# Kernel tuning notes

Hardware: AMD Instinct MI355X
Metric: run time of the kernel (lower is better)

Reference implementation:

```python
import jax, jax.numpy as jnp
import numpy as np

BATCH = 262144
N_STEPS = 10  # hard-coded `range(10)` in the original get_cycles


def _euler_to_matrix(e):
    # Standard extrinsic xyz convention: R = Rz(z) @ Ry(y) @ Rx(x)
    x, y, z = e[..., 0], e[..., 1], e[..., 2]
    cx, sx = jnp.cos(x), jnp.sin(x)
    cy, sy = jnp.cos(y), jnp.sin(y)
    cz, sz = jnp.cos(z), jnp.sin(z)
    r0 = jnp.stack([cz * cy, cz * sy * sx - sz * cx, cz * sy * cx + sz * sx], -1)
    r1 = jnp.stack([sz * cy, sz * sy * sx + cz * cx, sz * sy * cx - cz * sx], -1)
    r2 = jnp.stack([-sy, cy * sx, cy * cx], -1)
    return jnp.stack([r0, r1, r2], -2)  # (..., 3, 3)


def _matrix_to_euler(R):
    # Classic rotationMatrixToEulerAngles (inverse of Rz@Ry@Rx), with singular branch
    sy = jnp.sqrt(R[..., 0, 0] ** 2 + R[..., 1, 0] ** 2)
    singular = sy < 1e-6
    x = jnp.where(singular,
                  jnp.arctan2(-R[..., 1, 2], R[..., 1, 1]),
                  jnp.arctan2(R[..., 2, 1], R[..., 2, 2]))
    y = jnp.arctan2(-R[..., 2, 0], sy)
    z = jnp.where(singular, jnp.zeros_like(sy), jnp.arctan2(R[..., 1, 0], R[..., 0, 0]))
    return jnp.stack([x, y, z], -1)


def _get_cycles(x):
    # x: (B, 6*N_STEPS), interleaved [t(3), r(3)] per step (per the original reshape())
    x = jax.lax.stop_gradient(x)  # mirrors .detach().numpy() in the original
    g = x.reshape(x.shape[0], N_STEPS, 6)
    t = g[:, :, :3]   # (B, S, 3) translations
    r = g[:, :, 3:]   # (B, S, 3) euler rotations

    # --- translation part ---
    # The original aliases path_pred[0] onto t[0:3] via .numpy() and mutates it
    # in-place across cycle iterations (j=0 doubles it). The resulting recorded
    # values obey: v_0 = t_0 ; v_i = 2*v_{i-1} + sum_{j=1}^{i-1} t_j
    C = jnp.cumsum(t[:, 1:, :], axis=1)  # C[:, k-1, :] = sum_{j=1..k} t_j
    v = [t[:, 0, :]]
    for i in range(1, N_STEPS):
        tail = C[:, i - 2, :] if i >= 2 else jnp.zeros_like(v[0])
        v.append(2.0 * v[-1] + tail)
    trans = jnp.stack(v, axis=1)  # (B, S, 3)

    # --- rotation part ---
    # numpy `*=` is ELEMENTWISE, so cycle i records
    # matrix_to_euler( R(r_1) * prod_{j<i} R(r_j) )  (Hadamard product)
    R = _euler_to_matrix(r)                    # (B, S, 3, 3)
    CP = jnp.cumprod(R, axis=1)                # CP[:, k] = elemwise prod_{j<=k} R_j
    P = jnp.concatenate([jnp.ones_like(R[:, :1]), CP[:, :-1]], axis=1)  # prod_{j<i}
    M = R[:, 1:2] * P                          # (B, S, 3, 3)
    rot = _matrix_to_euler(M)                  # (B, S, 3)

    return jnp.stack([trans, rot], axis=2)     # (B, S, 2, 3)


def setup_inputs():
    key = jax.random.key(0)
    k1, k2 = jax.random.split(key)
    pred = jax.random.normal(k1, (BATCH, 6 * N_STEPS), dtype=jnp.float32)
    gt = jax.random.normal(k2, (BATCH, 6 * N_STEPS), dtype=jnp.float32)
    return {"pred": pred, "gt": gt}


def reference(pred, gt):
    pred_cycles = _get_cycles(pred)
    gt_cycles = _get_cycles(gt)
    loss = jnp.mean((pred_cycles - gt_cycles) ** 2)
    return loss / BATCH  # original divides the MSE by self.batch_size
```

## Files before the change

### kernel.cpp

```cpp
#include <hip/hip_runtime.h>
#include <math.h>

#define NSTEP 10

__device__ __forceinline__ float fast_atan2f(float y, float x) {
    float ax = fabsf(x), ay = fabsf(y);
    float mx = fmaxf(ax, ay);
    float mn = fminf(ax, ay);
    float a = mn * __builtin_amdgcn_rcpf(mx);
    float s = a * a;
    float r = fmaf(s, fmaf(s, 0.0793312f, -0.2886793f), 0.9953545f) * a;
    if (ay > ax) r = 1.57079632679f - r;
    if (x < 0.0f) r = 3.14159265359f - r;
    return copysignf(r, y);
}

__device__ __forceinline__ void euler2mat5(float x, float y, float z, float R[5]) {
    float sx, cx, sy, cy, sz, cz;
    __sincosf(x, &sx, &cx);
    __sincosf(y, &sy, &cy);
    __sincosf(z, &sz, &cz);
    R[0] = cz * cy;
    R[1] = sz * cy;
    R[2] = -sy;
    R[3] = cy * sx;
    R[4] = cy * cx;
}

__device__ __forceinline__ void emit(float v, float& acc) {
    int pi = __builtin_amdgcn_update_dpp(0, __float_as_int(v), 0xB1, 0xF, 0xF, true);
    float d = v - __int_as_float(pi);
    acc = fmaf(d, d, acc);
}

__device__ __forceinline__ void emit_euler(const float M[5], float& acc) {
    float sy = __builtin_amdgcn_sqrtf(fmaf(M[0], M[0], M[1] * M[1]));
    emit(fast_atan2f(M[3], M[4]), acc);
    emit(fast_atan2f(-M[2], sy), acc);
    emit(fast_atan2f(M[1], M[0]), acc);
}

__global__ __launch_bounds__(256, 8) void cycle_loss_main(
    const float* __restrict__ pred, const float* __restrict__ gt,
    float* __restrict__ partial)
{
    const int tid  = threadIdx.x;
    const int lane = tid & 63;
    const int wid  = tid >> 6;

    const size_t sample = (size_t)blockIdx.x * 128 + (tid >> 1);
    const float* bp = (tid & 1) ? gt : pred;
    const float4* rp = reinterpret_cast<const float4*>(bp + sample * 60);

    float acc = 0.0f;
    float v[3], cac[3] = {0.f, 0.f, 0.f}, tprev[3], Q[5];

    float4 A = rp[0], B = rp[1], C = rp[2];

    {
        float4 nA = rp[3], nB = rp[4], nC = rp[5];
        float e0 = A.x, e1 = A.y, e2 = A.z, e3 = A.w,
              e4 = B.x, e5 = B.y, e6 = B.z, e7 = B.w,
              e8 = C.x, e9 = C.y, e10 = C.z, e11 = C.w;

        v[0] = e0; v[1] = e1; v[2] = e2;
        emit(v[0], acc); emit(v[1], acc); emit(v[2], acc);
        #pragma unroll
        for (int k = 0; k < 3; ++k) { v[k] *= 2.0f; emit(v[k], acc); }
        tprev[0] = e6; tprev[1] = e7; tprev[2] = e8;

        float R1[5];
        euler2mat5(e3, e4, e5, Q);
        euler2mat5(e9, e10, e11, R1);
        emit_euler(R1, acc);
        #pragma unroll
        for (int k = 0; k < 5; ++k) Q[k] *= R1[k];
        emit_euler(Q, acc);
        #pragma unroll
        for (int k = 0; k < 5; ++k) Q[k] *= R1[k];

        A = nA; B = nB; C = nC;
    }

    #pragma unroll
    for (int c = 1; c < 5; ++c) {
        float4 nA, nB, nC;
        if (c < 4) { nA = rp[3*c + 3]; nB = rp[3*c + 4]; nC = rp[3*c + 5]; }
        float f0 = A.x, f1 = A.y, f2 = A.z, f3 = A.w,
              f4 = B.x, f5 = B.y, f6 = B.z, f7 = B.w,
              f8 = C.x, f9 = C.y, f10 = C.z, f11 = C.w;
        (void)f4; (void)f5;

        cac[0] += tprev[0]; cac[1] += tprev[1]; cac[2] += tprev[2];
        #pragma unroll
        for (int k = 0; k < 3; ++k) { v[k] = fmaf(2.0f, v[k], cac[k]); emit(v[k], acc); }
        cac[0] += f0; cac[1] += f1; cac[2] += f2;
        #pragma unroll
        for (int k = 0; k < 3; ++k) { v[k] = fmaf(2.0f, v[k], cac[k]); emit(v[k], acc); }
        tprev[0] = f6; tprev[1] = f7; tprev[2] = f8;

        emit_euler(Q, acc);
        {
            float R[5];
            euler2mat5(f3, f4, f5, R);
            #pragma unroll
            for (int k = 0; k < 5; ++k) Q[k] *= R[k];
        }
        emit_euler(Q, acc);
        if (c < 4) {
            float R[5];
            euler2mat5(f9, f10, f11, R);
            #pragma unroll
            for (int k = 0; k < 5; ++k) Q[k] *= R[k];
            A = nA; B = nB; C = nC;
        }
    }

    #pragma unroll
    for (int off = 32; off > 0; off >>= 1)
        acc += __shfl_down(acc, off, 64);
    if (lane == 0)
        partial[blockIdx.x * 4 + wid] = acc;
}

__global__ __launch_bounds__(256) void cycle_loss_fin(
    const float* __restrict__ partial, float* __restrict__ out,
    int nparts, float inv)
{
    int t = threadIdx.x;
    float s = 0.0f;
    for (int i = t; i < nparts; i += 256) s += partial[i];
    int lane = t & 63, wid = t >> 6;
    #pragma unroll
    for (int off = 32; off > 0; off >>= 1)
        s += __shfl_down(s, off, 64);
    __shared__ float warp_s[4];
    if (lane == 0) warp_s[wid] = s;
    __syncthreads();
    if (t == 0)
        out[0] = (warp_s[0] + warp_s[1] + warp_s[2] + warp_s[3]) * inv;
}

extern "C" void kernel_launch(void* const* d_in, const int* in_sizes, int n_in,
                              void* d_out, int out_size, void* d_ws, size_t ws_size,
                              hipStream_t stream) {
    const float* pred = (const float*)d_in[0];
    const float* gt   = (const float*)d_in[1];
    int batch = in_sizes[0] / 60;
    float* partial = (float*)d_ws;

    const int threads = 256;
    const int blocks = batch / 128;
    cycle_loss_main<<<blocks, threads, 0, stream>>>(pred, gt, partial);

    double inv = 0.5 / (60.0 * (double)batch * (double)batch);
    cycle_loss_fin<<<1, threads, 0, stream>>>(partial, (float*)d_out, blocks * 4, (float)inv);
}
```

Before: 153.7 us.

## Fuse main and finalize kernels via cooperative launch with grid sync

```diff
diff --git a/kernel.cpp b/kernel.cpp
--- a/kernel.cpp
+++ b/kernel.cpp
@@ -1,5 +1,8 @@
 #include <hip/hip_runtime.h>
+#include <hip/hip_cooperative_groups.h>
 #include <math.h>
+
+namespace cg = cooperative_groups;
 
 #define NSTEP 10
 
@@ -40,19 +43,14 @@
     emit(fast_atan2f(M[1], M[0]), acc);
 }
 
-__global__ __launch_bounds__(256, 8) void cycle_loss_main(
+__device__ __forceinline__ void do_work(
     const float* __restrict__ pred, const float* __restrict__ gt,
-    float* __restrict__ partial)
+    int w, int tid, float& acc)
 {
-    const int tid  = threadIdx.x;
-    const int lane = tid & 63;
-    const int wid  = tid >> 6;
-
-    const size_t sample = (size_t)blockIdx.x * 128 + (tid >> 1);
+    const size_t sample = (size_t)w * 128 + (tid >> 1);
     const float* bp = (tid & 1) ? gt : pred;
     const float4* rp = reinterpret_cast<const float4*>(bp + sample * 60);
 
-    float acc = 0.0f;
     float v[3], cac[3] = {0.f, 0.f, 0.f}, tprev[3], Q[5];
 
     float4 A = rp[0], B = rp[1], C = rp[2];
@@ -62,6 +60,7 @@
         float e0 = A.x, e1 = A.y, e2 = A.z, e3 = A.w,
               e4 = B.x, e5 = B.y, e6 = B.z, e7 = B.w,
               e8 = C.x, e9 = C.y, e10 = C.z, e11 = C.w;
+        (void)e4; (void)e5;
 
         v[0] = e0; v[1] = e1; v[2] = e2;
         emit(v[0], acc); emit(v[1], acc); emit(v[2], acc);
@@ -115,30 +114,44 @@
             A = nA; B = nB; C = nC;
         }
     }
+}
+
+__global__ __launch_bounds__(256, 8) void cycle_loss_fused(
+    const float* __restrict__ pred, const float* __restrict__ gt,
+    float* __restrict__ partial, float* __restrict__ out,
+    int nwork, float inv)
+{
+    const int tid  = threadIdx.x;
+    const int lane = tid & 63;
+    const int wid  = tid >> 6;
+
+    float acc = 0.0f;
+    for (int w = blockIdx.x; w < nwork; w += gridDim.x)
+        do_work(pred, gt, w, tid, acc);
 
     #pragma unroll
     for (int off = 32; off > 0; off >>= 1)
         acc += __shfl_down(acc, off, 64);
-    if (lane == 0)
-        partial[blockIdx.x * 4 + wid] = acc;
-}
+    __shared__ float wsum[4];
+    __shared__ float wsum2[4];
+    if (lane == 0) wsum[wid] = acc;
+    __syncthreads();
+    if (tid == 0)
+        partial[blockIdx.x] = wsum[0] + wsum[1] + wsum[2] + wsum[3];
 
-__global__ __launch_bounds__(256) void cycle_loss_fin(
-    const float* __restrict__ partial, float* __restrict__ out,
-    int nparts, float inv)
-{
-    int t = threadIdx.x;
-    float s = 0.0f;
-    for (int i = t; i < nparts; i += 256) s += partial[i];
-    int lane = t & 63, wid = t >> 6;
-    #pragma unroll
-    for (int off = 32; off > 0; off >>= 1)
-        s += __shfl_down(s, off, 64);
-    __shared__ float warp_s[4];
-    if (lane == 0) warp_s[wid] = s;
-    __syncthreads();
-    if (t == 0)
-        out[0] = (warp_s[0] + warp_s[1] + warp_s[2] + warp_s[3]) * inv;
+    cg::this_grid().sync();
+
+    if (blockIdx.x == 0) {
+        float s = 0.0f;
+        for (int i = tid; i < (int)gridDim.x; i += 256) s += partial[i];
+        #pragma unroll
+        for (int off = 32; off > 0; off >>= 1)
+            s += __shfl_down(s, off, 64);
+        if (lane == 0) wsum2[wid] = s;
+        __syncthreads();
+        if (tid == 0)
+            out[0] = (wsum2[0] + wsum2[1] + wsum2[2] + wsum2[3]) * inv;
+    }
 }
 
 extern "C" void kernel_launch(void* const* d_in, const int* in_sizes, int n_in,
@@ -147,12 +160,26 @@
     const float* pred = (const float*)d_in[0];
     const float* gt   = (const float*)d_in[1];
     int batch = in_sizes[0] / 60;
+    int nwork = batch / 128;
     float* partial = (float*)d_ws;
+    float* outp = (float*)d_out;
 
-    const int threads = 256;
-    const int blocks = batch / 128;
-    cycle_loss_main<<<blocks, threads, 0, stream>>>(pred, gt, partial);
+    static int maxblk = 0;
+    if (maxblk == 0) {
+        int perCU = 0, ncu = 0;
+        hipOccupancyMaxActiveBlocksPerMultiprocessor(
+            &perCU, reinterpret_cast<const void*>(cycle_loss_fused), 256, 0);
+        hipDeviceGetAttribute(&ncu, hipDeviceAttributeMultiprocessorCount, 0);
+        if (perCU < 1) perCU = 1;
+        if (ncu < 1) ncu = 256;
+        maxblk = perCU * ncu;
+    }
+    int blocks = maxblk < nwork ? maxblk : nwork;
 
-    double inv = 0.5 / (60.0 * (double)batch * (double)batch);
-    cycle_loss_fin<<<1, threads, 0, stream>>>(partial, (float*)d_out, blocks * 4, (float)inv);
+    float inv = (float)(0.5 / (60.0 * (double)batch * (double)batch));
+
+    void* args[] = { (void*)&pred, (void*)&gt, (void*)&partial,
+                     (void*)&outp, (void*)&nwork, (void*)&inv };
+    hipLaunchCooperativeKernel(reinterpret_cast<void*>(cycle_loss_fused),
+                               dim3(blocks), dim3(256), args, 0, stream);
 }
```

New measurement: 314.2 us. 104% more time.

## Stage sample rows into LDS via coalesced global_load_lds with one-wave blocks

Applied to the files above, without the earlier changes.

```diff
diff --git a/kernel.cpp b/kernel.cpp
--- a/kernel.cpp
+++ b/kernel.cpp
@@ -2,6 +2,11 @@
 #include <math.h>
 
 #define NSTEP 10
+#define TILE_DW   3840
+#define GT_DW     1920
+
+#define GV (const __attribute__((address_space(1))) void*)
+#define LV (__attribute__((address_space(3))) void*)
 
 __device__ __forceinline__ float fast_atan2f(float y, float x) {
     float ax = fabsf(x), ay = fabsf(y);
@@ -40,25 +45,38 @@
     emit(fast_atan2f(M[1], M[0]), acc);
 }
 
-__global__ __launch_bounds__(256, 8) void cycle_loss_main(
+__global__ __launch_bounds__(64, 4) void cycle_loss_main(
     const float* __restrict__ pred, const float* __restrict__ gt,
     float* __restrict__ partial)
 {
-    const int tid  = threadIdx.x;
-    const int lane = tid & 63;
-    const int wid  = tid >> 6;
+    __shared__ float lds[TILE_DW];
+    const int lane = threadIdx.x;
 
-    const size_t sample = (size_t)blockIdx.x * 128 + (tid >> 1);
-    const float* bp = (tid & 1) ? gt : pred;
-    const float4* rp = reinterpret_cast<const float4*>(bp + sample * 60);
+    {
+        const size_t base = (size_t)blockIdx.x * 32 * 60;
+        const float* pg = pred + base;
+        const float* gg = gt   + base;
+
+        #pragma unroll
+        for (int it = 0; it < 15; ++it) {
+            const int d = it * 256 + lane * 4;
+            const float* src = (d < GT_DW) ? (pg + d) : (gg + (d - GT_DW));
+            __builtin_amdgcn_global_load_lds(GV src, LV(lds + it * 256), 16, 0, 0);
+        }
+        asm volatile("s_waitcnt vmcnt(0)" ::: "memory");
+        __builtin_amdgcn_sched_barrier(0);
+    }
 
     float acc = 0.0f;
-    float v[3], cac[3] = {0.f, 0.f, 0.f}, tprev[3], Q[5];
+    {
+        const float* row = lds + ((lane & 1) ? GT_DW : 0) + (lane >> 1) * 60;
 
-    float4 A = rp[0], B = rp[1], C = rp[2];
+        float v[3], cac[3] = {0,0,0}, tprev[3];
+        float Q[5];
 
-    {
-        float4 nA = rp[3], nB = rp[4], nC = rp[5];
+        float4 A = *reinterpret_cast<const float4*>(row);
+        float4 B = *reinterpret_cast<const float4*>(row + 4);
+        float4 C = *reinterpret_cast<const float4*>(row + 8);
         float e0 = A.x, e1 = A.y, e2 = A.z, e3 = A.w,
               e4 = B.x, e5 = B.y, e6 = B.z, e7 = B.w,
               e8 = C.x, e9 = C.y, e10 = C.z, e11 = C.w;
@@ -69,50 +87,50 @@
         for (int k = 0; k < 3; ++k) { v[k] *= 2.0f; emit(v[k], acc); }
         tprev[0] = e6; tprev[1] = e7; tprev[2] = e8;
 
-        float R1[5];
-        euler2mat5(e3, e4, e5, Q);
-        euler2mat5(e9, e10, e11, R1);
-        emit_euler(R1, acc);
+        {
+            float R1[5];
+            euler2mat5(e3, e4, e5, Q);
+            euler2mat5(e9, e10, e11, R1);
+            emit_euler(R1, acc);
+            #pragma unroll
+            for (int k = 0; k < 5; ++k) Q[k] *= R1[k];
+            emit_euler(Q, acc);
+            #pragma unroll
+            for (int k = 0; k < 5; ++k) Q[k] *= R1[k];
+        }
+
         #pragma unroll
-        for (int k = 0; k < 5; ++k) Q[k] *= R1[k];
-        emit_euler(Q, acc);
-        #pragma unroll
-        for (int k = 0; k < 5; ++k) Q[k] *= R1[k];
+        for (int c = 1; c < 5; ++c) {
+            const float* rc = row + 12 * c;
+            float4 FA = *reinterpret_cast<const float4*>(rc);
+            float4 FB = *reinterpret_cast<const float4*>(rc + 4);
+            float4 FC = *reinterpret_cast<const float4*>(rc + 8);
+            float f0 = FA.x, f1 = FA.y, f2 = FA.z, f3 = FA.w,
+                  f4 = FB.x, f5 = FB.y, f6 = FB.z, f7 = FB.w,
+                  f8 = FC.x, f9 = FC.y, f10 = FC.z, f11 = FC.w;
 
-        A = nA; B = nB; C = nC;
-    }
+            cac[0] += tprev[0]; cac[1] += tprev[1]; cac[2] += tprev[2];
+            #pragma unroll
+            for (int k = 0; k < 3; ++k) { v[k] = fmaf(2.0f, v[k], cac[k]); emit(v[k], acc); }
+            cac[0] += f0; cac[1] += f1; cac[2] += f2;
+            #pragma unroll
+            for (int k = 0; k < 3; ++k) { v[k] = fmaf(2.0f, v[k], cac[k]); emit(v[k], acc); }
+            tprev[0] = f6; tprev[1] = f7; tprev[2] = f8;
 
-    #pragma unroll
-    for (int c = 1; c < 5; ++c) {
-        float4 nA, nB, nC;
-        if (c < 4) { nA = rp[3*c + 3]; nB = rp[3*c + 4]; nC = rp[3*c + 5]; }
-        float f0 = A.x, f1 = A.y, f2 = A.z, f3 = A.w,
-              f4 = B.x, f5 = B.y, f6 = B.z, f7 = B.w,
-              f8 = C.x, f9 = C.y, f10 = C.z, f11 = C.w;
-        (void)f4; (void)f5;
-
-        cac[0] += tprev[0]; cac[1] += tprev[1]; cac[2] += tprev[2];
-        #pragma unroll
-        for (int k = 0; k < 3; ++k) { v[k] = fmaf(2.0f, v[k], cac[k]); emit(v[k], acc); }
-        cac[0] += f0; cac[1] += f1; cac[2] += f2;
-        #pragma unroll
-        for (int k = 0; k < 3; ++k) { v[k] = fmaf(2.0f, v[k], cac[k]); emit(v[k], acc); }
-        tprev[0] = f6; tprev[1] = f7; tprev[2] = f8;
-
-        emit_euler(Q, acc);
-        {
-            float R[5];
-            euler2mat5(f3, f4, f5, R);
-            #pragma unroll
-            for (int k = 0; k < 5; ++k) Q[k] *= R[k];
-        }
-        emit_euler(Q, acc);
-        if (c < 4) {
-            float R[5];
-            euler2mat5(f9, f10, f11, R);
-            #pragma unroll
-            for (int k = 0; k < 5; ++k) Q[k] *= R[k];
-            A = nA; B = nB; C = nC;
+            emit_euler(Q, acc);
+            {
+                float R[5];
+                euler2mat5(f3, f4, f5, R);
+                #pragma unroll
+                for (int k = 0; k < 5; ++k) Q[k] *= R[k];
+            }
+            emit_euler(Q, acc);
+            if (c < 4) {
+                float R[5];
+                euler2mat5(f9, f10, f11, R);
+                #pragma unroll
+                for (int k = 0; k < 5; ++k) Q[k] *= R[k];
+            }
         }
     }
 
@@ -120,7 +138,7 @@
     for (int off = 32; off > 0; off >>= 1)
         acc += __shfl_down(acc, off, 64);
     if (lane == 0)
-        partial[blockIdx.x * 4 + wid] = acc;
+        partial[blockIdx.x] = acc;
 }
 
 __global__ __launch_bounds__(256) void cycle_loss_fin(
@@ -149,10 +167,9 @@
     int batch = in_sizes[0] / 60;
     float* partial = (float*)d_ws;
 
-    const int threads = 256;
-    const int blocks = batch / 128;
-    cycle_loss_main<<<blocks, threads, 0, stream>>>(pred, gt, partial);
+    const int blocks = batch / 32;
+    cycle_loss_main<<<blocks, 64, 0, stream>>>(pred, gt, partial);
 
     double inv = 0.5 / (60.0 * (double)batch * (double)batch);
-    cycle_loss_fin<<<1, threads, 0, stream>>>(partial, (float*)d_out, blocks * 4, (float)inv);
+    cycle_loss_fin<<<1, 256, 0, stream>>>(partial, (float*)d_out, blocks, (float)inv);
 }
```

Result: faster. 146.5 us (-4.7%).
